# Performance work log

Measured on AMD Instinct MI355X. Metric: run time of the kernel, lower is better.

The kernel has to match this reference:

```python
import jax, jax.numpy as jnp
import numpy as np

B, POOL, PACK = 4096, 45, 15
E, D, V = 512, 8, 30000  # embedding_dim, internal_dims, num_cards
SQRT_D = float(np.sqrt(D))


def setup_inputs() -> dict:
    key = jax.random.key(0)
    ks = jax.random.split(key, 12)
    s = 0.02
    return {
        "pool": jax.random.randint(ks[0], (B, POOL), 0, V),
        "pack": jax.random.randint(ks[1], (B, PACK), 0, V),
        "wins": jax.random.uniform(ks[2], (B,), dtype=jnp.float32),
        "ranks": jax.random.uniform(ks[3], (B,), dtype=jnp.float32),
        "emb_table": jax.random.normal(ks[4], (V, E), dtype=jnp.float32) * s,
        "win_w": jax.random.normal(ks[5], (E, 1), dtype=jnp.float32) * s,
        "win_b": jnp.zeros((E,), dtype=jnp.float32),
        "rank_w": jax.random.normal(ks[6], (E, 1), dtype=jnp.float32) * s,
        "rank_b": jnp.zeros((E,), dtype=jnp.float32),
        "q_w": jax.random.normal(ks[7], (D, E), dtype=jnp.float32) * s,
        "k_w": jax.random.normal(ks[8], (D, E), dtype=jnp.float32) * s,
        "v_w": jax.random.normal(ks[9], (D, E), dtype=jnp.float32) * s,
        "sc_w": jax.random.normal(ks[10], (1, D), dtype=jnp.float32) * s,
        "sc_b": jnp.zeros((1,), dtype=jnp.float32),
    }


def reference(pool, pack, wins, ranks, emb_table, win_w, win_b,
              rank_w, rank_b, q_w, k_w, v_w, sc_w, sc_b):
    pool_emb = emb_table[pool]                                   # [B, POOL, E]
    pack_emb = emb_table[pack]                                   # [B, PACK, E]
    win_emb = wins[:, None, None] * win_w[:, 0] + win_b          # [B, 1, E]
    rank_emb = ranks[:, None, None] * rank_w[:, 0] + rank_b      # [B, 1, E]
    pool_full = jnp.concatenate([pool_emb, win_emb, rank_emb], axis=1)  # [B, POOL+2, E]
    pool_full = jax.nn.relu(pool_full)
    q = jnp.einsum("bke,de->bkd", pack_emb, q_w)                 # [B, PACK, D]
    k = jnp.einsum("bpe,de->bpd", pool_full, k_w)                # [B, POOL+2, D]
    v = jnp.einsum("bpe,de->bpd", pool_full, v_w)                # [B, POOL+2, D]
    scores = jnp.einsum("bkd,bpd->bkp", q, k) / SQRT_D
    attn = jax.nn.softmax(jax.nn.relu(scores), axis=-1)          # [B, PACK, POOL+2]
    context = jnp.einsum("bkp,bpd->bkd", attn, v)                # [B, PACK, D]
    context = jax.nn.leaky_relu(context, negative_slope=0.01)
    logits = jnp.einsum("bkd,od->bko", context, sc_w) + sc_b     # [B, PACK, 1]
    return logits[..., 0]                                        # [B, PACK]
```

## Files before the change

kernel.cpp:

```cpp
#include <hip/hip_runtime.h>

#define B_N 4096
#define POOL_N 45
#define PACK_N 15
#define E_N 512
#define D_N 8
#define V_N 30000

#define WT_SZ  (E_N * 24)
#define TAB_SZ (V_N * 24)

__global__ __launch_bounds__(256) void k_transpose_w(const float* __restrict__ q_w,
                                                     const float* __restrict__ k_w,
                                                     const float* __restrict__ v_w,
                                                     float* __restrict__ wt) {
  int i = blockIdx.x * 256 + threadIdx.x;
  if (i >= E_N * 24) return;
  int e = i / 24, j = i % 24;
  float val = (j < 8) ? q_w[j * E_N + e]
            : (j < 16) ? k_w[(j - 8) * E_N + e]
                       : v_w[(j - 16) * E_N + e];
  wt[i] = val;
}

__global__ __launch_bounds__(512) void k_build_tab(const float* __restrict__ emb,
                                                   const float* __restrict__ wt,
                                                   float* __restrict__ tab) {
  __shared__ float red[8][64][25];
  int lane = threadIdx.x & 63;
  int w = __builtin_amdgcn_readfirstlane(threadIdx.x >> 6);
  int r = blockIdx.x * 64 + lane;
  float acc[24];
#pragma unroll
  for (int j = 0; j < 24; ++j) acc[j] = 0.f;
  if (r < V_N) {
    const float* a = emb + (size_t)r * E_N + w * 64;
    const float* wp = wt + (w * 64) * 24;
#pragma unroll 4
    for (int i = 0; i < 16; ++i) {
      float4 av = ((const float4*)a)[i];
      float xs[4] = {av.x, av.y, av.z, av.w};
#pragma unroll
      for (int c = 0; c < 4; ++c) {
        float x = xs[c];
        float xr = fmaxf(x, 0.f);
        const float* wr = wp + (i * 4 + c) * 24;
#pragma unroll
        for (int j = 0; j < 8; ++j) acc[j] = fmaf(x, wr[j], acc[j]);
#pragma unroll
        for (int j = 8; j < 24; ++j) acc[j] = fmaf(xr, wr[j], acc[j]);
      }
    }
  }
#pragma unroll
  for (int j = 0; j < 24; ++j) red[w][lane][j] = acc[j];
  __syncthreads();
  int t = threadIdx.x;
#pragma unroll
  for (int i = 0; i < 3; ++i) {
    int o = t + 512 * i;
    int row = o / 24, col = o - row * 24;
    int r_out = blockIdx.x * 64 + row;
    if (r_out < V_N) {
      float v = 0.f;
#pragma unroll
      for (int s = 0; s < 8; ++s) v += red[s][row][col];
      tab[(size_t)r_out * 24 + col] = v;
    }
  }
}

__global__ __launch_bounds__(256) void k_build_aux(const float* __restrict__ wins,
                                                   const float* __restrict__ ranks,
                                                   const float* __restrict__ win_w,
                                                   const float* __restrict__ win_b,
                                                   const float* __restrict__ rank_w,
                                                   const float* __restrict__ rank_b,
                                                   const float* __restrict__ wt,
                                                   float* __restrict__ aux) {
  __shared__ float red[16][16][17];
  int t = threadIdx.x;
  int bl = t & 15, seg = t >> 4;
  int which = blockIdx.y;
  int b = blockIdx.x * 16 + bl;
  float s = which ? ranks[b] : wins[b];
  const float* ww = which ? rank_w : win_w;
  const float* wb = which ? rank_b : win_b;
  float acc[16];
#pragma unroll
  for (int j = 0; j < 16; ++j) acc[j] = 0.f;
  int e0 = seg * 32;
#pragma unroll 4
  for (int e = e0; e < e0 + 32; ++e) {
    float x = fmaf(s, ww[e], wb[e]);
    float xr = fmaxf(x, 0.f);
    const float* wr = wt + e * 24 + 8;
#pragma unroll
    for (int j = 0; j < 16; ++j) acc[j] = fmaf(xr, wr[j], acc[j]);
  }
#pragma unroll
  for (int j = 0; j < 16; ++j) red[seg][bl][j] = acc[j];
  __syncthreads();
  int bi = t >> 4, j = t & 15;
  float v = 0.f;
#pragma unroll
  for (int sg = 0; sg < 16; ++sg) v += red[sg][bi][j];
  aux[(size_t)(blockIdx.x * 16 + bi) * 32 + which * 16 + j] = v;
}

__global__ __launch_bounds__(256) void k_main(const int* __restrict__ pool,
                                              const int* __restrict__ pack,
                                              const float* __restrict__ tab,
                                              const float* __restrict__ aux,
                                              const float* __restrict__ sc_w,
                                              const float* __restrict__ sc_b,
                                              float* __restrict__ out) {
  int grp = threadIdx.x >> 5;
  int lane = threadIdx.x & 31;
  int b = blockIdx.x * 8 + grp;
  int i0 = pool[(size_t)b * POOL_N + lane];
  int i1 = (lane < POOL_N - 32) ? pool[(size_t)b * POOL_N + 32 + lane] : 0;
  int k = (lane < PACK_N) ? lane : 0;
  int qidx = pack[(size_t)b * PACK_N + k];
  const float* qr = tab + (size_t)qidx * 24;
  float4 qa = *(const float4*)qr;
  float4 qb = *(const float4*)(qr + 4);
  const float rs = 0.35355339059327373f;
  const float* auxb = aux + (size_t)b * 32;

  float m = 0.f, sum = 0.f;
  float ctx[8] = {0.f, 0.f, 0.f, 0.f, 0.f, 0.f, 0.f, 0.f};

  auto att_step = [&](const float* kr) {
    float4 k0 = *(const float4*)kr;
    float4 k1 = *(const float4*)(kr + 4);
    float4 v0 = *(const float4*)(kr + 8);
    float4 v1 = *(const float4*)(kr + 12);
    float d = qa.x * k0.x;
    d = fmaf(qa.y, k0.y, d);
    d = fmaf(qa.z, k0.z, d);
    d = fmaf(qa.w, k0.w, d);
    d = fmaf(qb.x, k1.x, d);
    d = fmaf(qb.y, k1.y, d);
    d = fmaf(qb.z, k1.z, d);
    d = fmaf(qb.w, k1.w, d);
    d = fmaxf(d * rs, 0.f);
    float t = __expf(-fabsf(d - m));
    bool up = d > m;
    float sc = up ? t : 1.f;
    float e = up ? 1.f : t;
    m = fmaxf(m, d);
    sum = fmaf(sum, sc, e);
    ctx[0] = fmaf(ctx[0], sc, e * v0.x);
    ctx[1] = fmaf(ctx[1], sc, e * v0.y);
    ctx[2] = fmaf(ctx[2], sc, e * v0.z);
    ctx[3] = fmaf(ctx[3], sc, e * v0.w);
    ctx[4] = fmaf(ctx[4], sc, e * v1.x);
    ctx[5] = fmaf(ctx[5], sc, e * v1.y);
    ctx[6] = fmaf(ctx[6], sc, e * v1.z);
    ctx[7] = fmaf(ctx[7], sc, e * v1.w);
  };

#pragma unroll 8
  for (int p = 0; p < 32; ++p) {
    int pi = __shfl(i0, p, 32);
    att_step(tab + (size_t)pi * 24 + 8);
  }
#pragma unroll
  for (int p = 0; p < 13; ++p) {
    int pi = __shfl(i1, p, 32);
    att_step(tab + (size_t)pi * 24 + 8);
  }
  att_step(auxb);
  att_step(auxb + 16);

  float inv = 1.f / sum;
  float logit = 0.f;
#pragma unroll
  for (int d0 = 0; d0 < 8; ++d0) {
    float c = ctx[d0] * inv;
    c = (c > 0.f) ? c : 0.01f * c;
    logit = fmaf(c, sc_w[d0], logit);
  }
  logit += sc_b[0];
  if (lane < PACK_N) out[(size_t)b * PACK_N + lane] = logit;
}

extern "C" void kernel_launch(void* const* d_in, const int* in_sizes, int n_in,
                              void* d_out, int out_size, void* d_ws, size_t ws_size,
                              hipStream_t stream) {
  const int* pool = (const int*)d_in[0];
  const int* pack = (const int*)d_in[1];
  const float* wins = (const float*)d_in[2];
  const float* ranks = (const float*)d_in[3];
  const float* emb = (const float*)d_in[4];
  const float* win_w = (const float*)d_in[5];
  const float* win_b = (const float*)d_in[6];
  const float* rank_w = (const float*)d_in[7];
  const float* rank_b = (const float*)d_in[8];
  const float* q_w = (const float*)d_in[9];
  const float* k_w = (const float*)d_in[10];
  const float* v_w = (const float*)d_in[11];
  const float* sc_w = (const float*)d_in[12];
  const float* sc_b = (const float*)d_in[13];

  float* ws = (float*)d_ws;
  float* wt = ws;
  float* tab = ws + WT_SZ;
  float* aux = ws + WT_SZ + TAB_SZ;
  float* out = (float*)d_out;

  hipLaunchKernelGGL(k_transpose_w, dim3(48), dim3(256), 0, stream,
                     q_w, k_w, v_w, wt);
  hipLaunchKernelGGL(k_build_tab, dim3((V_N + 63) / 64), dim3(512), 0, stream,
                     emb, wt, tab);
  hipLaunchKernelGGL(k_build_aux, dim3(B_N / 16, 2), dim3(256), 0, stream,
                     wins, ranks, win_w, win_b, rank_w, rank_b, wt, aux);
  hipLaunchKernelGGL(k_main, dim3(B_N / 8), dim3(256), 0, stream,
                     pool, pack, tab, aux, sc_w, sc_b, out);
}
```

Before: 53.83 us.

## Stage embedding tiles through LDS with coalesced loads in table-build kernel

The projected-table kernel now loads 64 rows × 128 columns of the embedding table per iteration with coalesced float4 loads and writes them transposed into LDS. Each of four waves then reduces a 32-column slice for all 64 rows. This replaces the old per-lane strided row reads, which were poorly coalesced. The block shrinks from 512 to 256 threads with a 4-way instead of 8-way final reduction, at the cost of extra barriers and a larger LDS footprint per block.

Measured after the change: 61.23 us. +13.7%, slower.

```diff
diff --git a/kernel.cpp b/kernel.cpp
--- a/kernel.cpp
+++ b/kernel.cpp
@@ -9,6 +9,7 @@
 
 #define WT_SZ  (E_N * 24)
 #define TAB_SZ (V_N * 24)
+#define AUX_SZ (B_N * 32)
 
 __global__ __launch_bounds__(256) void k_transpose_w(const float* __restrict__ q_w,
                                                      const float* __restrict__ k_w,
@@ -23,48 +24,56 @@
   wt[i] = val;
 }
 
-__global__ __launch_bounds__(512) void k_build_tab(const float* __restrict__ emb,
+__global__ __launch_bounds__(256) void k_build_tab(const float* __restrict__ emb,
                                                    const float* __restrict__ wt,
                                                    float* __restrict__ tab) {
-  __shared__ float red[8][64][25];
-  int lane = threadIdx.x & 63;
-  int w = __builtin_amdgcn_readfirstlane(threadIdx.x >> 6);
-  int r = blockIdx.x * 64 + lane;
+  __shared__ float lds[128 * 65];
+  int t = threadIdx.x;
+  int lane = t & 63;
+  int w = __builtin_amdgcn_readfirstlane(t >> 6);
+  int row0 = blockIdx.x * 64;
+  int f4 = t & 31;
+  int sr0 = t >> 5;
   float acc[24];
 #pragma unroll
   for (int j = 0; j < 24; ++j) acc[j] = 0.f;
-  if (r < V_N) {
-    const float* a = emb + (size_t)r * E_N + w * 64;
-    const float* wp = wt + (w * 64) * 24;
-#pragma unroll 4
-    for (int i = 0; i < 16; ++i) {
-      float4 av = ((const float4*)a)[i];
-      float xs[4] = {av.x, av.y, av.z, av.w};
-#pragma unroll
-      for (int c = 0; c < 4; ++c) {
-        float x = xs[c];
-        float xr = fmaxf(x, 0.f);
-        const float* wr = wp + (i * 4 + c) * 24;
-#pragma unroll
-        for (int j = 0; j < 8; ++j) acc[j] = fmaf(x, wr[j], acc[j]);
-#pragma unroll
-        for (int j = 8; j < 24; ++j) acc[j] = fmaf(xr, wr[j], acc[j]);
-      }
+
+  for (int it = 0; it < 4; ++it) {
+    int eb = it * 128;
+    __syncthreads();
+#pragma unroll
+    for (int sub = 0; sub < 8; ++sub) {
+      int sr = sub * 8 + sr0;
+      int gr = row0 + sr;
+      if (gr > V_N - 1) gr = V_N - 1;
+      float4 v = *(const float4*)(emb + (size_t)gr * E_N + eb + f4 * 4);
+      float* d = lds + (f4 * 4) * 65 + sr;
+      d[0] = v.x; d[65] = v.y; d[130] = v.z; d[195] = v.w;
     }
-  }
-#pragma unroll
-  for (int j = 0; j < 24; ++j) red[w][lane][j] = acc[j];
+    __syncthreads();
+    const float* wp = wt + (size_t)(eb + w * 32) * 24;
+    const float* ep = lds + (w * 32) * 65 + lane;
+#pragma unroll
+    for (int el = 0; el < 32; ++el) {
+      float x = ep[el * 65];
+      float xr = fmaxf(x, 0.f);
+      const float* wr = wp + el * 24;
+#pragma unroll
+      for (int j = 0; j < 8; ++j) acc[j] = fmaf(x, wr[j], acc[j]);
+#pragma unroll
+      for (int j = 8; j < 24; ++j) acc[j] = fmaf(xr, wr[j], acc[j]);
+    }
+  }
   __syncthreads();
-  int t = threadIdx.x;
-#pragma unroll
-  for (int i = 0; i < 3; ++i) {
-    int o = t + 512 * i;
+#pragma unroll
+  for (int j = 0; j < 24; ++j) lds[w * 1600 + lane * 25 + j] = acc[j];
+  __syncthreads();
+  for (int o = t; o < 1536; o += 256) {
     int row = o / 24, col = o - row * 24;
-    int r_out = blockIdx.x * 64 + row;
+    int r_out = row0 + row;
     if (r_out < V_N) {
-      float v = 0.f;
-#pragma unroll
-      for (int s = 0; s < 8; ++s) v += red[s][row][col];
+      float v = lds[row * 25 + col] + lds[1600 + row * 25 + col]
+              + lds[3200 + row * 25 + col] + lds[4800 + row * 25 + col];
       tab[(size_t)r_out * 24 + col] = v;
     }
   }
@@ -212,7 +221,7 @@
 
   hipLaunchKernelGGL(k_transpose_w, dim3(48), dim3(256), 0, stream,
                      q_w, k_w, v_w, wt);
-  hipLaunchKernelGGL(k_build_tab, dim3((V_N + 63) / 64), dim3(512), 0, stream,
+  hipLaunchKernelGGL(k_build_tab, dim3((V_N + 63) / 64), dim3(256), 0, stream,
                      emb, wt, tab);
   hipLaunchKernelGGL(k_build_aux, dim3(B_N / 16, 2), dim3(256), 0, stream,
                      wins, ranks, win_w, win_b, rank_w, rank_b, wt, aux);
```

## Fuse all stages into one cooperative persistent kernel with grid syncs

Applied to the files above, without the earlier changes.

Replaces the four separate launches (weight transpose, table build, aux build, main attention) with a single cooperative kernel of 256 blocks of 512 threads that uses grid.sync between phases. Each block builds 128 table rows instead of 64, and the aux computation now reads k_w/v_w directly instead of the transposed buffer. The aim is to remove launch gaps and inter-kernel drain. In exchange, the table build runs on only 256 blocks, which limits parallelism, grid-wide barriers add cost, and a fallback three-kernel path covers the case where the cooperative launch fails.

Measured after the change: 135.0 us. +150.8%, slower.

```diff
diff --git a/kernel.cpp b/kernel.cpp
--- a/kernel.cpp
+++ b/kernel.cpp
@@ -1,123 +1,74 @@
 #include <hip/hip_runtime.h>
+#include <hip/hip_cooperative_groups.h>
+
+namespace cg = cooperative_groups;
 
 #define B_N 4096
 #define POOL_N 45
 #define PACK_N 15
 #define E_N 512
-#define D_N 8
 #define V_N 30000
 
 #define WT_SZ  (E_N * 24)
 #define TAB_SZ (V_N * 24)
-
-__global__ __launch_bounds__(256) void k_transpose_w(const float* __restrict__ q_w,
-                                                     const float* __restrict__ k_w,
-                                                     const float* __restrict__ v_w,
-                                                     float* __restrict__ wt) {
-  int i = blockIdx.x * 256 + threadIdx.x;
-  if (i >= E_N * 24) return;
-  int e = i / 24, j = i % 24;
-  float val = (j < 8) ? q_w[j * E_N + e]
-            : (j < 16) ? k_w[(j - 8) * E_N + e]
-                       : v_w[(j - 16) * E_N + e];
-  wt[i] = val;
-}
-
-__global__ __launch_bounds__(512) void k_build_tab(const float* __restrict__ emb,
-                                                   const float* __restrict__ wt,
-                                                   float* __restrict__ tab) {
-  __shared__ float red[8][64][25];
-  int lane = threadIdx.x & 63;
-  int w = __builtin_amdgcn_readfirstlane(threadIdx.x >> 6);
-  int r = blockIdx.x * 64 + lane;
-  float acc[24];
-#pragma unroll
-  for (int j = 0; j < 24; ++j) acc[j] = 0.f;
-  if (r < V_N) {
-    const float* a = emb + (size_t)r * E_N + w * 64;
-    const float* wp = wt + (w * 64) * 24;
-#pragma unroll 4
-    for (int i = 0; i < 16; ++i) {
-      float4 av = ((const float4*)a)[i];
-      float xs[4] = {av.x, av.y, av.z, av.w};
-#pragma unroll
-      for (int c = 0; c < 4; ++c) {
-        float x = xs[c];
-        float xr = fmaxf(x, 0.f);
-        const float* wr = wp + (i * 4 + c) * 24;
-#pragma unroll
-        for (int j = 0; j < 8; ++j) acc[j] = fmaf(x, wr[j], acc[j]);
-#pragma unroll
-        for (int j = 8; j < 24; ++j) acc[j] = fmaf(xr, wr[j], acc[j]);
-      }
-    }
-  }
-#pragma unroll
-  for (int j = 0; j < 24; ++j) red[w][lane][j] = acc[j];
-  __syncthreads();
-  int t = threadIdx.x;
-#pragma unroll
-  for (int i = 0; i < 3; ++i) {
-    int o = t + 512 * i;
-    int row = o / 24, col = o - row * 24;
-    int r_out = blockIdx.x * 64 + row;
-    if (r_out < V_N) {
+#define AUX_SZ (B_N * 32)
+
+
+__device__ __forceinline__ void body_pre(int blk, int t,
+    const float* __restrict__ wins, const float* __restrict__ ranks,
+    const float* __restrict__ win_w, const float* __restrict__ win_b,
+    const float* __restrict__ rank_w, const float* __restrict__ rank_b,
+    const float* __restrict__ q_w, const float* __restrict__ k_w,
+    const float* __restrict__ v_w,
+    float* __restrict__ wt, float* __restrict__ aux, float* lds) {
+  if (blk < 24) {
+    int i = blk * 512 + t;
+    int e = i / 24, j = i % 24;
+    float val = (j < 8) ? q_w[j * E_N + e]
+              : (j < 16) ? k_w[(j - 8) * E_N + e]
+                         : v_w[(j - 16) * E_N + e];
+    wt[i] = val;
+  }
+  int bl = t & 15, seg = t >> 4;
+  int b = blk * 16 + bl;
+  for (int which = 0; which < 2; ++which) {
+    float s = which ? ranks[b] : wins[b];
+    const float* ww = which ? rank_w : win_w;
+    const float* wb = which ? rank_b : win_b;
+    float acc[16];
+#pragma unroll
+    for (int j = 0; j < 16; ++j) acc[j] = 0.f;
+    int e0 = seg * 16;
+    for (int e = e0; e < e0 + 16; ++e) {
+      float x = fmaf(s, ww[e], wb[e]);
+      float xr = fmaxf(x, 0.f);
+#pragma unroll
+      for (int j = 0; j < 8; ++j) acc[j] = fmaf(xr, k_w[j * E_N + e], acc[j]);
+#pragma unroll
+      for (int j = 0; j < 8; ++j) acc[8 + j] = fmaf(xr, v_w[j * E_N + e], acc[8 + j]);
+    }
+#pragma unroll
+    for (int j = 0; j < 16; ++j) lds[(seg * 16 + bl) * 17 + j] = acc[j];
+    __syncthreads();
+    if (t < 256) {
+      int bi = t >> 4, jj = t & 15;
       float v = 0.f;
 #pragma unroll
-      for (int s = 0; s < 8; ++s) v += red[s][row][col];
-      tab[(size_t)r_out * 24 + col] = v;
-    }
-  }
-}
-
-__global__ __launch_bounds__(256) void k_build_aux(const float* __restrict__ wins,
-                                                   const float* __restrict__ ranks,
-                                                   const float* __restrict__ win_w,
-                                                   const float* __restrict__ win_b,
-                                                   const float* __restrict__ rank_w,
-                                                   const float* __restrict__ rank_b,
-                                                   const float* __restrict__ wt,
-                                                   float* __restrict__ aux) {
-  __shared__ float red[16][16][17];
-  int t = threadIdx.x;
-  int bl = t & 15, seg = t >> 4;
-  int which = blockIdx.y;
-  int b = blockIdx.x * 16 + bl;
-  float s = which ? ranks[b] : wins[b];
-  const float* ww = which ? rank_w : win_w;
-  const float* wb = which ? rank_b : win_b;
-  float acc[16];
-#pragma unroll
-  for (int j = 0; j < 16; ++j) acc[j] = 0.f;
-  int e0 = seg * 32;
-#pragma unroll 4
-  for (int e = e0; e < e0 + 32; ++e) {
-    float x = fmaf(s, ww[e], wb[e]);
-    float xr = fmaxf(x, 0.f);
-    const float* wr = wt + e * 24 + 8;
-#pragma unroll
-    for (int j = 0; j < 16; ++j) acc[j] = fmaf(xr, wr[j], acc[j]);
-  }
-#pragma unroll
-  for (int j = 0; j < 16; ++j) red[seg][bl][j] = acc[j];
-  __syncthreads();
-  int bi = t >> 4, j = t & 15;
-  float v = 0.f;
-#pragma unroll
-  for (int sg = 0; sg < 16; ++sg) v += red[sg][bi][j];
-  aux[(size_t)(blockIdx.x * 16 + bi) * 32 + which * 16 + j] = v;
-}
-
-__global__ __launch_bounds__(256) void k_main(const int* __restrict__ pool,
-                                              const int* __restrict__ pack,
-                                              const float* __restrict__ tab,
-                                              const float* __restrict__ aux,
-                                              const float* __restrict__ sc_w,
-                                              const float* __restrict__ sc_b,
-                                              float* __restrict__ out) {
-  int grp = threadIdx.x >> 5;
-  int lane = threadIdx.x & 31;
-  int b = blockIdx.x * 8 + grp;
+      for (int sg = 0; sg < 32; ++sg) v += lds[(sg * 16 + bi) * 17 + jj];
+      aux[(size_t)(blk * 16 + bi) * 32 + which * 16 + jj] = v;
+    }
+    __syncthreads();
+  }
+}
+
+__device__ __forceinline__ void body_main(int blk, int t,
+    const int* __restrict__ pool, const int* __restrict__ pack,
+    const float* __restrict__ tab, const float* __restrict__ aux,
+    const float* __restrict__ sc_w, const float* __restrict__ sc_b,
+    float* __restrict__ out) {
+  int grp = t >> 5;
+  int lane = t & 31;
+  int b = blk * 16 + grp;
   int i0 = pool[(size_t)b * POOL_N + lane];
   int i1 = (lane < POOL_N - 32) ? pool[(size_t)b * POOL_N + 32 + lane] : 0;
   int k = (lane < PACK_N) ? lane : 0;
@@ -145,10 +96,10 @@
     d = fmaf(qb.z, k1.z, d);
     d = fmaf(qb.w, k1.w, d);
     d = fmaxf(d * rs, 0.f);
-    float t = __expf(-fabsf(d - m));
+    float tt = __expf(-fabsf(d - m));
     bool up = d > m;
-    float sc = up ? t : 1.f;
-    float e = up ? 1.f : t;
+    float sc = up ? tt : 1.f;
+    float e = up ? 1.f : tt;
     m = fmaxf(m, d);
     sum = fmaf(sum, sc, e);
     ctx[0] = fmaf(ctx[0], sc, e * v0.x);
@@ -184,6 +135,160 @@
   }
   logit += sc_b[0];
   if (lane < PACK_N) out[(size_t)b * PACK_N + lane] = logit;
+}
+
+__global__ __launch_bounds__(512) void k_fused(
+    const int* __restrict__ pool, const int* __restrict__ pack,
+    const float* __restrict__ wins, const float* __restrict__ ranks,
+    const float* __restrict__ emb,
+    const float* __restrict__ win_w, const float* __restrict__ win_b,
+    const float* __restrict__ rank_w, const float* __restrict__ rank_b,
+    const float* __restrict__ q_w, const float* __restrict__ k_w,
+    const float* __restrict__ v_w,
+    const float* __restrict__ sc_w, const float* __restrict__ sc_b,
+    float* __restrict__ wt, float* __restrict__ tab,
+    float* __restrict__ aux, float* __restrict__ out) {
+  cg::grid_group grid = cg::this_grid();
+  __shared__ float lds[12800];
+  int t = threadIdx.x;
+  int blk = blockIdx.x;
+
+  body_pre(blk, t, wins, ranks, win_w, win_b, rank_w, rank_b,
+           q_w, k_w, v_w, wt, aux, lds);
+  grid.sync();
+
+  {
+    int lane = t & 63;
+    int w = t >> 6;
+    int r0 = blk * 128 + lane;
+    int r1 = r0 + 64;
+    int c0 = (r0 < V_N) ? r0 : V_N - 1;
+    int c1 = (r1 < V_N) ? r1 : V_N - 1;
+    const float* a0 = emb + (size_t)c0 * E_N + w * 64;
+    const float* a1 = emb + (size_t)c1 * E_N + w * 64;
+    const float* wp = wt + (w * 64) * 24;
+    float acc0[24], acc1[24];
+#pragma unroll
+    for (int j = 0; j < 24; ++j) { acc0[j] = 0.f; acc1[j] = 0.f; }
+#pragma unroll 4
+    for (int i = 0; i < 16; ++i) {
+      float4 av0 = ((const float4*)a0)[i];
+      float4 av1 = ((const float4*)a1)[i];
+      float xs0[4] = {av0.x, av0.y, av0.z, av0.w};
+      float xs1[4] = {av1.x, av1.y, av1.z, av1.w};
+#pragma unroll
+      for (int c = 0; c < 4; ++c) {
+        const float* wr = wp + (i * 4 + c) * 24;
+        float x0 = xs0[c], xr0 = fmaxf(x0, 0.f);
+        float x1 = xs1[c], xr1 = fmaxf(x1, 0.f);
+#pragma unroll
+        for (int j = 0; j < 8; ++j) {
+          acc0[j] = fmaf(x0, wr[j], acc0[j]);
+          acc1[j] = fmaf(x1, wr[j], acc1[j]);
+        }
+#pragma unroll
+        for (int j = 8; j < 24; ++j) {
+          acc0[j] = fmaf(xr0, wr[j], acc0[j]);
+          acc1[j] = fmaf(xr1, wr[j], acc1[j]);
+        }
+      }
+    }
+    __syncthreads();
+#pragma unroll
+    for (int j = 0; j < 24; ++j) lds[w * 1600 + lane * 25 + j] = acc0[j];
+    __syncthreads();
+    for (int o = t; o < 1536; o += 512) {
+      int row = o / 24, col = o - row * 24;
+      int r_out = blk * 128 + row;
+      if (r_out < V_N) {
+        float v = 0.f;
+#pragma unroll
+        for (int s = 0; s < 8; ++s) v += lds[s * 1600 + row * 25 + col];
+        tab[(size_t)r_out * 24 + col] = v;
+      }
+    }
+    __syncthreads();
+#pragma unroll
+    for (int j = 0; j < 24; ++j) lds[w * 1600 + lane * 25 + j] = acc1[j];
+    __syncthreads();
+    for (int o = t; o < 1536; o += 512) {
+      int row = o / 24, col = o - row * 24;
+      int r_out = blk * 128 + 64 + row;
+      if (r_out < V_N) {
+        float v = 0.f;
+#pragma unroll
+        for (int s = 0; s < 8; ++s) v += lds[s * 1600 + row * 25 + col];
+        tab[(size_t)r_out * 24 + col] = v;
+      }
+    }
+  }
+  grid.sync();
+
+  body_main(blk, t, pool, pack, tab, aux, sc_w, sc_b, out);
+}
+
+__global__ __launch_bounds__(512) void k_pre_fb(
+    const float* __restrict__ wins, const float* __restrict__ ranks,
+    const float* __restrict__ win_w, const float* __restrict__ win_b,
+    const float* __restrict__ rank_w, const float* __restrict__ rank_b,
+    const float* __restrict__ q_w, const float* __restrict__ k_w,
+    const float* __restrict__ v_w,
+    float* __restrict__ wt, float* __restrict__ aux) {
+  __shared__ float lds[12800];
+  body_pre(blockIdx.x, threadIdx.x, wins, ranks, win_w, win_b, rank_w, rank_b,
+           q_w, k_w, v_w, wt, aux, lds);
+}
+
+__global__ __launch_bounds__(512) void k_tab_fb(const float* __restrict__ emb,
+                                                const float* __restrict__ wt,
+                                                float* __restrict__ tab) {
+  __shared__ float red[8][64][25];
+  int lane = threadIdx.x & 63;
+  int w = threadIdx.x >> 6;
+  int r = blockIdx.x * 64 + lane;
+  float acc[24];
+#pragma unroll
+  for (int j = 0; j < 24; ++j) acc[j] = 0.f;
+  if (r < V_N) {
+    const float* a = emb + (size_t)r * E_N + w * 64;
+    const float* wp = wt + (w * 64) * 24;
+#pragma unroll 4
+    for (int i = 0; i < 16; ++i) {
+      float4 av = ((const float4*)a)[i];
+      float xs[4] = {av.x, av.y, av.z, av.w};
+#pragma unroll
+      for (int c = 0; c < 4; ++c) {
+        float x = xs[c];
+        float xr = fmaxf(x, 0.f);
+        const float* wr = wp + (i * 4 + c) * 24;
+#pragma unroll
+        for (int j = 0; j < 8; ++j) acc[j] = fmaf(x, wr[j], acc[j]);
+#pragma unroll
+        for (int j = 8; j < 24; ++j) acc[j] = fmaf(xr, wr[j], acc[j]);
+      }
+    }
+  }
+#pragma unroll
+  for (int j = 0; j < 24; ++j) red[w][lane][j] = acc[j];
+  __syncthreads();
+  for (int o = threadIdx.x; o < 1536; o += 512) {
+    int row = o / 24, col = o - row * 24;
+    int r_out = blockIdx.x * 64 + row;
+    if (r_out < V_N) {
+      float v = 0.f;
+#pragma unroll
+      for (int s = 0; s < 8; ++s) v += red[s][row][col];
+      tab[(size_t)r_out * 24 + col] = v;
+    }
+  }
+}
+
+__global__ __launch_bounds__(512) void k_main_fb(
+    const int* __restrict__ pool, const int* __restrict__ pack,
+    const float* __restrict__ tab, const float* __restrict__ aux,
+    const float* __restrict__ sc_w, const float* __restrict__ sc_b,
+    float* __restrict__ out) {
+  body_main(blockIdx.x, threadIdx.x, pool, pack, tab, aux, sc_w, sc_b, out);
 }
 
 extern "C" void kernel_launch(void* const* d_in, const int* in_sizes, int n_in,
@@ -210,12 +315,21 @@
   float* aux = ws + WT_SZ + TAB_SZ;
   float* out = (float*)d_out;
 
-  hipLaunchKernelGGL(k_transpose_w, dim3(48), dim3(256), 0, stream,
-                     q_w, k_w, v_w, wt);
-  hipLaunchKernelGGL(k_build_tab, dim3((V_N + 63) / 64), dim3(512), 0, stream,
-                     emb, wt, tab);
-  hipLaunchKernelGGL(k_build_aux, dim3(B_N / 16, 2), dim3(256), 0, stream,
-                     wins, ranks, win_w, win_b, rank_w, rank_b, wt, aux);
-  hipLaunchKernelGGL(k_main, dim3(B_N / 8), dim3(256), 0, stream,
-                     pool, pack, tab, aux, sc_w, sc_b, out);
-}
+  void* kargs[] = {(void*)&pool, (void*)&pack, (void*)&wins, (void*)&ranks,
+                   (void*)&emb, (void*)&win_w, (void*)&win_b, (void*)&rank_w,
+                   (void*)&rank_b, (void*)&q_w, (void*)&k_w, (void*)&v_w,
+                   (void*)&sc_w, (void*)&sc_b, (void*)&wt, (void*)&tab,
+                   (void*)&aux, (void*)&out};
+  hipError_t err = hipLaunchCooperativeKernel((const void*)k_fused, dim3(256),
+                                              dim3(512), kargs, 0, stream);
+  if (err != hipSuccess) {
+    (void)hipGetLastError();
+    hipLaunchKernelGGL(k_pre_fb, dim3(256), dim3(512), 0, stream,
+                       wins, ranks, win_w, win_b, rank_w, rank_b,
+                       q_w, k_w, v_w, wt, aux);
+    hipLaunchKernelGGL(k_tab_fb, dim3((V_N + 63) / 64), dim3(512), 0, stream,
+                       emb, wt, tab);
+    hipLaunchKernelGGL(k_main_fb, dim3(256), dim3(512), 0, stream,
+                       pool, pack, tab, aux, sc_w, sc_b, out);
+  }
+}
```
